# Optimization experiments

Hardware: AMD Instinct MI355X
Metric: run time of the kernel (lower is better)

## Reference

```python
import jax, jax.numpy as jnp
import numpy as np

KNN = 16


def _knn_idx(k, ref_xyz, query_xyz):
    # squared euclidean distances: (B, Nq, Nr)
    q2 = jnp.sum(query_xyz * query_xyz, axis=-1, keepdims=True)        # (B, Nq, 1)
    r2 = jnp.sum(ref_xyz * ref_xyz, axis=-1)[:, None, :]               # (B, 1, Nr)
    cross = jnp.einsum('bqc,brc->bqr', query_xyz, ref_xyz)             # (B, Nq, Nr)
    dist = q2 + r2 - 2.0 * cross
    neg_vals, idx = jax.lax.top_k(-dist, k)                            # k smallest dists
    return -neg_vals, idx


def setup_inputs() -> dict:
    key = jax.random.key(0)
    k1, k2, k3, k4 = jax.random.split(key, 4)
    B, N_prev, N_cur, C = 1, 8192, 4096, 256
    return {
        'xyz_prev': jax.random.normal(k1, (B, N_prev, 3), dtype=jnp.float32),
        'xyz_cur': jax.random.normal(k2, (B, N_cur, 3), dtype=jnp.float32),
        'feat_prev': jax.random.normal(k3, (B, N_prev, C), dtype=jnp.float32),
        'feat_cur': jax.random.normal(k4, (B, N_cur, C), dtype=jnp.float32),
    }


def reference(xyz_prev, xyz_cur, feat_prev, feat_cur):
    k = KNN
    _, idx = _knn_idx(k, xyz_prev, xyz_cur)                 # (B, Nq, k) per-batch-local indices
    B, Nq, _ = idx.shape
    C = feat_prev.shape[-1]
    idx_flat = idx.reshape(-1, k).astype(jnp.int32)          # (B*Nq, k)
    prev_flat = feat_prev.reshape(-1, C)                     # (B*Nprev, C)
    cur_flat = feat_cur.reshape(-1, C)                       # (B*Nq, C)
    # faithful to original: gather from flattened table with local indices (batch_dims=0)
    prev_sel = prev_flat[idx_flat]                           # (B*Nq, k, C)
    cur_sel = jnp.broadcast_to(cur_flat[:, None, :], (B * Nq, k, C))
    inter = jnp.concatenate([prev_sel - cur_sel, cur_sel], axis=-1)  # (B*Nq, k, 2C)
    return inter.reshape(B, Nq * k, 2 * C)
```

## Files before the change

kernel.cpp:

```cpp
#include <hip/hip_runtime.h>
#include <stdint.h>

#define KNN 16

typedef float vfloat4 __attribute__((ext_vector_type(4)));

__device__ __forceinline__ uint32_t fkey(float f) {
    uint32_t u = __float_as_uint(f);
    return (u & 0x80000000u) ? ~u : (u | 0x80000000u);
}

__global__ __launch_bounds__(256) void prep_kernel(
    const float* __restrict__ xyz_prev, vfloat4* __restrict__ P, int n_prev)
{
    const int i = blockIdx.x * 256 + threadIdx.x;
    if (i >= n_prev) return;
    const float x = xyz_prev[3 * i + 0];
    const float y = xyz_prev[3 * i + 1];
    const float z = xyz_prev[3 * i + 2];
    const float r2 = __fadd_rn(__fadd_rn(__fmul_rn(x, x), __fmul_rn(y, y)),
                               __fmul_rn(z, z));
    vfloat4 v = {x, y, z, r2};
    P[i] = v;
}

__global__ __launch_bounds__(256) void knn_kernel(
    const vfloat4* __restrict__ P, const float* __restrict__ xyz_cur,
    int* __restrict__ knn_idx, int n_prev, int n_cur)
{
    const int lane = threadIdx.x & 63;
    const int q = blockIdx.x * 4 + (threadIdx.x >> 6);
    if (q >= n_cur) return;

    const float qx = xyz_cur[3 * q + 0];
    const float qy = xyz_cur[3 * q + 1];
    const float qz = xyz_cur[3 * q + 2];
    const float q2 = __fadd_rn(__fadd_rn(__fmul_rn(qx, qx), __fmul_rn(qy, qy)),
                               __fmul_rn(qz, qz));

    unsigned long long v;
    {
        const int r = lane;
        const vfloat4 p = P[r < n_prev ? r : 0];
        const float cr = __fmaf_rn(p.z, qz, __fmaf_rn(p.y, qy, __fmul_rn(p.x, qx)));
        const float dist = __fsub_rn(__fadd_rn(q2, p.w), __fmul_rn(2.0f, cr));
        v = (r < n_prev)
            ? (((unsigned long long)fkey(dist) << 32) | (uint32_t)r)
            : ~0ull;
    }
#pragma unroll
    for (int k = 2; k <= 64; k <<= 1) {
#pragma unroll
        for (int j = k >> 1; j > 0; j >>= 1) {
            const unsigned long long o = __shfl_xor(v, j, 64);
            const bool keepMin = (((lane & k) == 0) == ((lane & j) == 0));
            const bool omin = o < v;
            v = (keepMin == omin) ? o : v;
        }
    }
    unsigned long long lkey = (lane < KNN) ? v : ~0ull;
    unsigned long long tau = __shfl(lkey, 15, 64);

    const int n_iter = (n_prev + 63) >> 6;
    int t = 1;
    for (; t + 7 < n_iter; t += 8) {
        vfloat4 pv[8];
#pragma unroll
        for (int u = 0; u < 8; ++u) {
            const int r = ((t + u) << 6) + lane;
            pv[u] = P[r < n_prev ? r : 0];
        }
#pragma unroll
        for (int u = 0; u < 8; ++u) {
            const int r = ((t + u) << 6) + lane;
            const vfloat4 p = pv[u];
            const float cr = __fmaf_rn(p.z, qz, __fmaf_rn(p.y, qy, __fmul_rn(p.x, qx)));
            const float dist = __fsub_rn(__fadd_rn(q2, p.w), __fmul_rn(2.0f, cr));
            const unsigned long long key = (r < n_prev)
                ? (((unsigned long long)fkey(dist) << 32) | (uint32_t)r)
                : ~0ull;
            unsigned long long mask = __ballot(key < tau);
            while (mask) {
                const int b = (int)__builtin_ctzll(mask);
                mask &= mask - 1;
                const unsigned long long bk = __shfl(key, b, 64);
                if (bk < tau) {
                    const unsigned long long sh = __shfl_up(lkey, 1, 64);
                    unsigned long long nk;
                    if (lkey < bk) nk = lkey;
                    else nk = (lane == 0 || sh < bk) ? bk : sh;
                    if (lane < KNN) lkey = nk;
                    tau = __shfl(lkey, 15, 64);
                }
            }
        }
    }
    for (; t < n_iter; ++t) {
        const int r = (t << 6) + lane;
        const vfloat4 p = P[r < n_prev ? r : 0];
        const float cr = __fmaf_rn(p.z, qz, __fmaf_rn(p.y, qy, __fmul_rn(p.x, qx)));
        const float dist = __fsub_rn(__fadd_rn(q2, p.w), __fmul_rn(2.0f, cr));
        const unsigned long long key = (r < n_prev)
            ? (((unsigned long long)fkey(dist) << 32) | (uint32_t)r)
            : ~0ull;
        unsigned long long mask = __ballot(key < tau);
        while (mask) {
            const int b = (int)__builtin_ctzll(mask);
            mask &= mask - 1;
            const unsigned long long bk = __shfl(key, b, 64);
            if (bk < tau) {
                const unsigned long long sh = __shfl_up(lkey, 1, 64);
                unsigned long long nk;
                if (lkey < bk) nk = lkey;
                else nk = (lane == 0 || sh < bk) ? bk : sh;
                if (lane < KNN) lkey = nk;
                tau = __shfl(lkey, 15, 64);
            }
        }
    }

    if (lane < KNN)
        knn_idx[q * KNN + lane] = (int)(lkey & 0xffffffffu);
}

__global__ __launch_bounds__(256) void combine_kernel(
    const float* __restrict__ feat_prev, const float* __restrict__ feat_cur,
    const int* __restrict__ knn_idx, float* __restrict__ out,
    int n_cur, int c4)
{
    const int w = blockIdx.x * 4 + (threadIdx.x >> 6);
    const int lane = threadIdx.x & 63;
    const int q = w >> 2;
    const int jg = (w & 3) * 4;
    if (q >= n_cur) return;

    int nb[4];
#pragma unroll
    for (int j = 0; j < 4; ++j)
        nb[j] = knn_idx[q * KNN + jg + j];

    const vfloat4* pbase = (const vfloat4*)feat_prev;
    const vfloat4* crow  = (const vfloat4*)feat_cur + (size_t)q * c4;
    const int c8 = 2 * c4;

    for (int i = lane; i < c4; i += 64) {
        const vfloat4 c = crow[i];
        vfloat4 p[4];
#pragma unroll
        for (int j = 0; j < 4; ++j)
            p[j] = pbase[(size_t)nb[j] * c4 + i];

#pragma unroll
        for (int j = 0; j < 4; ++j) {
            vfloat4* orow = (vfloat4*)out + (size_t)(q * KNN + jg + j) * c8;
            __builtin_nontemporal_store(p[j] - c, orow + i);
            __builtin_nontemporal_store(c, orow + c4 + i);
        }
    }
}

extern "C" void kernel_launch(void* const* d_in, const int* in_sizes, int n_in,
                              void* d_out, int out_size, void* d_ws, size_t ws_size,
                              hipStream_t stream) {
    const float* xyz_prev  = (const float*)d_in[0];
    const float* xyz_cur   = (const float*)d_in[1];
    const float* feat_prev = (const float*)d_in[2];
    const float* feat_cur  = (const float*)d_in[3];
    float* out = (float*)d_out;

    const int n_prev = in_sizes[0] / 3;
    const int n_cur  = in_sizes[1] / 3;
    const int C      = in_sizes[2] / n_prev;

    vfloat4* P = (vfloat4*)d_ws;
    int* knn = (int*)((char*)d_ws + (size_t)n_prev * sizeof(vfloat4));

    prep_kernel<<<(n_prev + 255) / 256, 256, 0, stream>>>(xyz_prev, P, n_prev);

    const int knn_blocks = (n_cur + 3) / 4;
    knn_kernel<<<knn_blocks, 256, 0, stream>>>(P, xyz_cur, knn, n_prev, n_cur);

    const int n_waves = n_cur * 4;
    combine_kernel<<<(n_waves + 3) / 4, 256, 0, stream>>>(feat_prev, feat_cur,
                                                          knn, out, n_cur, C / 4);
}
```

Before: 207.5 us.

## Stage reference points through LDS tiles shared by the block's four query waves

```diff
diff --git a/kernel.cpp b/kernel.cpp
--- a/kernel.cpp
+++ b/kernel.cpp
@@ -2,6 +2,7 @@
 #include <stdint.h>
 
 #define KNN 16
+#define CHUNK 2048
 
 typedef float vfloat4 __attribute__((ext_vector_type(4)));
 
@@ -28,52 +29,94 @@
     const vfloat4* __restrict__ P, const float* __restrict__ xyz_cur,
     int* __restrict__ knn_idx, int n_prev, int n_cur)
 {
+    __shared__ vfloat4 tile[CHUNK];
     const int lane = threadIdx.x & 63;
     const int q = blockIdx.x * 4 + (threadIdx.x >> 6);
-    if (q >= n_cur) return;
-
-    const float qx = xyz_cur[3 * q + 0];
-    const float qy = xyz_cur[3 * q + 1];
-    const float qz = xyz_cur[3 * q + 2];
+    const bool active = (q < n_cur);
+    const int qc = active ? q : (n_cur - 1);
+
+    const float qx = xyz_cur[3 * qc + 0];
+    const float qy = xyz_cur[3 * qc + 1];
+    const float qz = xyz_cur[3 * qc + 2];
     const float q2 = __fadd_rn(__fadd_rn(__fmul_rn(qx, qx), __fmul_rn(qy, qy)),
                                __fmul_rn(qz, qz));
 
-    unsigned long long v;
-    {
-        const int r = lane;
-        const vfloat4 p = P[r < n_prev ? r : 0];
-        const float cr = __fmaf_rn(p.z, qz, __fmaf_rn(p.y, qy, __fmul_rn(p.x, qx)));
-        const float dist = __fsub_rn(__fadd_rn(q2, p.w), __fmul_rn(2.0f, cr));
-        v = (r < n_prev)
-            ? (((unsigned long long)fkey(dist) << 32) | (uint32_t)r)
-            : ~0ull;
-    }
-#pragma unroll
-    for (int k = 2; k <= 64; k <<= 1) {
-#pragma unroll
-        for (int j = k >> 1; j > 0; j >>= 1) {
-            const unsigned long long o = __shfl_xor(v, j, 64);
-            const bool keepMin = (((lane & k) == 0) == ((lane & j) == 0));
-            const bool omin = o < v;
-            v = (keepMin == omin) ? o : v;
-        }
-    }
-    unsigned long long lkey = (lane < KNN) ? v : ~0ull;
-    unsigned long long tau = __shfl(lkey, 15, 64);
-
-    const int n_iter = (n_prev + 63) >> 6;
-    int t = 1;
-    for (; t + 7 < n_iter; t += 8) {
-        vfloat4 pv[8];
-#pragma unroll
-        for (int u = 0; u < 8; ++u) {
-            const int r = ((t + u) << 6) + lane;
-            pv[u] = P[r < n_prev ? r : 0];
-        }
-#pragma unroll
-        for (int u = 0; u < 8; ++u) {
-            const int r = ((t + u) << 6) + lane;
-            const vfloat4 p = pv[u];
+    unsigned long long lkey = ~0ull;
+    unsigned long long tau = ~0ull;
+    bool warmed = false;
+
+    const int n_chunks = (n_prev + CHUNK - 1) / CHUNK;
+    for (int chunk = 0; chunk < n_chunks; ++chunk) {
+        const int base = chunk * CHUNK;
+#pragma unroll
+        for (int k = 0; k < CHUNK / 256; ++k) {
+            const int li = (k << 8) + threadIdx.x;
+            const int gi = base + li;
+            tile[li] = P[gi < n_prev ? gi : 0];
+        }
+        __syncthreads();
+
+        const int iters = (CHUNK + 63) >> 6;
+        int i0 = 0;
+
+        if (!warmed) {
+            const int r = base + lane;
+            const vfloat4 p = tile[lane];
+            const float cr = __fmaf_rn(p.z, qz, __fmaf_rn(p.y, qy, __fmul_rn(p.x, qx)));
+            const float dist = __fsub_rn(__fadd_rn(q2, p.w), __fmul_rn(2.0f, cr));
+            unsigned long long v = (r < n_prev)
+                ? (((unsigned long long)fkey(dist) << 32) | (uint32_t)r)
+                : ~0ull;
+#pragma unroll
+            for (int k = 2; k <= 64; k <<= 1) {
+#pragma unroll
+                for (int j = k >> 1; j > 0; j >>= 1) {
+                    const unsigned long long o = __shfl_xor(v, j, 64);
+                    const bool keepMin = (((lane & k) == 0) == ((lane & j) == 0));
+                    const bool omin = o < v;
+                    v = (keepMin == omin) ? o : v;
+                }
+            }
+            lkey = (lane < KNN) ? v : ~0ull;
+            tau = __shfl(lkey, 15, 64);
+            warmed = true;
+            i0 = 1;
+        }
+
+        int i = i0;
+        for (; i + 3 < iters; i += 4) {
+            vfloat4 pv[4];
+#pragma unroll
+            for (int u = 0; u < 4; ++u)
+                pv[u] = tile[((i + u) << 6) + lane];
+#pragma unroll
+            for (int u = 0; u < 4; ++u) {
+                const int r = base + ((i + u) << 6) + lane;
+                const vfloat4 p = pv[u];
+                const float cr = __fmaf_rn(p.z, qz, __fmaf_rn(p.y, qy, __fmul_rn(p.x, qx)));
+                const float dist = __fsub_rn(__fadd_rn(q2, p.w), __fmul_rn(2.0f, cr));
+                const unsigned long long key = (r < n_prev)
+                    ? (((unsigned long long)fkey(dist) << 32) | (uint32_t)r)
+                    : ~0ull;
+                unsigned long long mask = __ballot(key < tau);
+                while (mask) {
+                    const int b = (int)__builtin_ctzll(mask);
+                    mask &= mask - 1;
+                    const unsigned long long bk = __shfl(key, b, 64);
+                    if (bk < tau) {
+                        const unsigned long long sh = __shfl_up(lkey, 1, 64);
+                        unsigned long long nk;
+                        if (lkey < bk) nk = lkey;
+                        else nk = (lane == 0 || sh < bk) ? bk : sh;
+                        if (lane < KNN) lkey = nk;
+                        tau = __shfl(lkey, 15, 64);
+                    }
+                }
+            }
+        }
+        for (; i < iters; ++i) {
+            const int r = base + (i << 6) + lane;
+            const vfloat4 p = tile[(i << 6) + lane];
             const float cr = __fmaf_rn(p.z, qz, __fmaf_rn(p.y, qy, __fmul_rn(p.x, qx)));
             const float dist = __fsub_rn(__fadd_rn(q2, p.w), __fmul_rn(2.0f, cr));
             const unsigned long long key = (r < n_prev)
@@ -94,32 +137,10 @@
                 }
             }
         }
+        __syncthreads();
     }
-    for (; t < n_iter; ++t) {
-        const int r = (t << 6) + lane;
-        const vfloat4 p = P[r < n_prev ? r : 0];
-        const float cr = __fmaf_rn(p.z, qz, __fmaf_rn(p.y, qy, __fmul_rn(p.x, qx)));
-        const float dist = __fsub_rn(__fadd_rn(q2, p.w), __fmul_rn(2.0f, cr));
-        const unsigned long long key = (r < n_prev)
-            ? (((unsigned long long)fkey(dist) << 32) | (uint32_t)r)
-            : ~0ull;
-        unsigned long long mask = __ballot(key < tau);
-        while (mask) {
-            const int b = (int)__builtin_ctzll(mask);
-            mask &= mask - 1;
-            const unsigned long long bk = __shfl(key, b, 64);
-            if (bk < tau) {
-                const unsigned long long sh = __shfl_up(lkey, 1, 64);
-                unsigned long long nk;
-                if (lkey < bk) nk = lkey;
-                else nk = (lane == 0 || sh < bk) ? bk : sh;
-                if (lane < KNN) lkey = nk;
-                tau = __shfl(lkey, 15, 64);
-            }
-        }
-    }
-
-    if (lane < KNN)
+
+    if (active && lane < KNN)
         knn_idx[q * KNN + lane] = (int)(lkey & 0xffffffffu);
 }
 
```

After: 210.4 us. Within noise of the previous version (+1.4%).
